# Optimization experiments

Measured on AMD Instinct MI355X. Metric: run time of the kernel, lower is better.

Reference implementation:

```python
import jax, jax.numpy as jnp
import numpy as np

J = 25
C_IN, HID, LAT = 3, 64, 32


def _graph_conv(x, A, W, b):
    # x: [N,T,J,Cin]; A: [J,J]; W: [Cin,Cout]; b: [Cout]
    A = jax.nn.softmax(A, axis=-1)
    # fused adjacency mix + projection: (A @ x) @ W + b
    x = jnp.einsum('ij,ntjc->ntic', A, x)
    return jnp.einsum('ntjc,cd->ntjd', x, W) + b


def setup_inputs() -> dict:
    key = jax.random.key(0)
    ks = jax.random.split(key, 13)
    x = jax.random.normal(ks[0], (32, 2048, J, C_IN), dtype=jnp.float32)
    eye = jnp.eye(J, dtype=jnp.float32)
    def lin(kw, kb, cin, cout):
        W = jax.random.normal(kw, (cin, cout), dtype=jnp.float32) / np.sqrt(cin)
        b = jax.random.normal(kb, (cout,), dtype=jnp.float32) * 0.01
        return W, b
    W1, b1 = lin(ks[1], ks[2], C_IN, HID)
    W2, b2 = lin(ks[3], ks[4], HID, LAT)
    W3, b3 = lin(ks[5], ks[6], LAT, HID)
    W4, b4 = lin(ks[7], ks[8], HID, C_IN)
    return {
        'x': x,
        'A1': eye, 'W1': W1, 'b1': b1,
        'A2': eye, 'W2': W2, 'b2': b2,
        'A3': eye, 'W3': W3, 'b3': b3,
        'A4': eye, 'W4': W4, 'b4': b4,
    }


def reference(x, A1, W1, b1, A2, W2, b2, A3, W3, b3, A4, W4, b4):
    h = jax.nn.relu(_graph_conv(x, A1, W1, b1))     # encoder_g1 + relu
    z = _graph_conv(h, A2, W2, b2)                  # encoder_g2 (no relu)
    h_dec = jax.nn.relu(_graph_conv(z, A3, W3, b3)) # decoder_g1 + relu
    out = _graph_conv(h_dec, A4, W4, b4)            # decoder_g2
    return out
```

## Files before the change

### kernel.cpp

```cpp
#include <hip/hip_runtime.h>
#include <math.h>

#define J 25
#define NJC 75
#define NWAVE 4
#define NTHREADS 256
#define NFPW 4
#define SCRW 2112

#define O_A1T  0
#define O_APP  1024
#define O_A4B  2048
#define O_W2T  3072
#define O_W3T  5120
#define O_W1T  7168
#define O_W4C  8192
#define O_B4   8512
#define O_BPPF 8576

using bf16x2 = __attribute__((ext_vector_type(2))) __bf16;
using bf16x8 = __attribute__((ext_vector_type(8))) __bf16;
using f32x4  = __attribute__((ext_vector_type(4))) float;
using f32x16 = __attribute__((ext_vector_type(16))) float;

__device__ inline bf16x8 zero8() {
    bf16x8 z;
    #pragma unroll
    for (int j = 0; j < 8; j++) z[j] = (__bf16)0.f;
    return z;
}

#if defined(__has_builtin)
#if __has_builtin(__builtin_amdgcn_cvt_pk_bf16_f32)
#define HAVE_PK_BF16 1
#endif
#endif

__device__ inline bf16x2 cvt2(float a, float b) {
#ifdef HAVE_PK_BF16
    return __builtin_amdgcn_cvt_pk_bf16_f32(a, b);
#else
    bf16x2 r; r[0] = (__bf16)a; r[1] = (__bf16)b; return r;
#endif
}
__device__ inline bf16x8 pk8(const f32x16& acc, int st) {
    const int b = 8 * st;
    bf16x8 r;
    #pragma unroll
    for (int p = 0; p < 4; p++) {
        bf16x2 v = cvt2(acc[b + 2 * p], acc[b + 2 * p + 1]);
        r[2 * p] = v[0]; r[2 * p + 1] = v[1];
    }
    return r;
}


__global__ void gcn_precompute(
    const float* __restrict__ A1, const float* __restrict__ W1, const float* __restrict__ b1,
    const float* __restrict__ A2, const float* __restrict__ W2, const float* __restrict__ b2,
    const float* __restrict__ A3, const float* __restrict__ W3, const float* __restrict__ b3,
    const float* __restrict__ A4, const float* __restrict__ W4, const float* __restrict__ b4,
    __bf16* __restrict__ cw)
{
    __shared__ float T[3125];
    __shared__ float bpp[64];
    float* T0 = T;        float* T1 = T + 625;  float* T2 = T + 1250;
    float* T3 = T + 1875; float* T4 = T + 2500;
    const int t = threadIdx.x;

    if (t < 100) {
        const int m = t / J, i = t % J;
        const float* Asrc = (m == 0) ? A1 : (m == 1) ? A2 : (m == 2) ? A3 : A4;
        float row[J];
        float mx = -1e30f;
        #pragma unroll
        for (int j = 0; j < J; j++) { row[j] = Asrc[i * J + j]; mx = fmaxf(mx, row[j]); }
        float s = 0.f;
        #pragma unroll
        for (int j = 0; j < J; j++) { row[j] = __expf(row[j] - mx); s += row[j]; }
        const float inv = 1.f / s;
        float* dst = T + m * 625 + i * J;
        #pragma unroll
        for (int j = 0; j < J; j++) dst[j] = row[j] * inv;
    }
    if (t < 64) {
        float s = b3[t];
        #pragma unroll
        for (int l = 0; l < 32; l++) s += W3[l * 64 + t] * b2[l];
        bpp[t] = s;
    }
    __syncthreads();

    for (int idx = t; idx < 625; idx += 256) {
        const int i = idx / J, jj = idx % J;
        float s = 0.f;
        #pragma unroll
        for (int k = 0; k < J; k++) s += T2[i * J + k] * T1[k * J + jj];
        T4[idx] = s;
    }
    __syncthreads();

    for (int i = t; i < 1024; i += 256) {
        const int b = i >> 8, n = (i >> 3) & 31, jj = i & 7;
        const int kn = 8 * b + jj;
        cw[O_A1T + i] = (__bf16)((kn < J && n < J) ? T0[n * J + kn] : 0.f);
        const int s = b >> 1, h = b & 1, r = 8 * s + jj;
        const int k32 = (r & 3) + 8 * (r >> 2) + 4 * h;
        cw[O_APP + i] = (__bf16)((k32 < J && n < J) ? T4[n * J + k32] : 0.f);
        cw[O_A4B + i] = (__bf16)((k32 < J && n < J) ? T3[n * J + k32] : 0.f);
    }
    for (int i = t; i < 2048; i += 256) {
        {
            const int b = i >> 8, n = (i >> 3) & 31, jj = i & 7;
            const int s = b >> 1, h = b & 1, r = 8 * (s & 1) + jj;
            const int d = 32 * (s >> 1) + (r & 3) + 8 * (r >> 2) + 4 * h;
            cw[O_W2T + i] = (__bf16)W2[d * 32 + n];
        }
        {
            const int tt = i >> 10, rr = i & 1023;
            const int b = rr >> 8, m = (rr >> 3) & 31, jj = rr & 7;
            const int s = b >> 1, h = b & 1, r = 8 * s + jj;
            const int l = (r & 3) + 8 * (r >> 2) + 4 * h;
            cw[O_W3T + i] = (__bf16)W3[l * 64 + tt * 32 + m];
        }
    }
    for (int i = t; i < 1024; i += 256) {
        const int tt = i >> 9, r = i & 511, hf = r >> 8, q = r & 255;
        const int m = q >> 3, c = q & 7, d = tt * 32 + m;
        float v = 0.f;
        if (hf == 0) {
            if (c < 3) v = W1[c * 64 + d];
            else if (c == 3) v = b1[d];
        }
        cw[O_W1T + i] = (__bf16)v;
    }
    if (t < 256) {
        const int c = t >> 6, b = (t >> 3) & 7, jj = t & 7;
        const int s = b >> 1, h = b & 1, r = 8 * (s & 1) + jj;
        const int d = 32 * (s >> 1) + (r & 3) + 8 * (r >> 2) + 4 * h;
        cw[O_W4C + t] = (c < 3) ? (__bf16)W4[d * 3 + c] : (__bf16)0.f;
    }
    {
        float* fwB = (float*)(cw + O_BPPF);
        if (t < 64) {
            const int g = t >> 4, h = (t >> 3) & 1, jj = t & 7;
            const int tt = g >> 1, st = g & 1;
            const int row32 = (jj & 3) + 16 * st + 8 * (jj >> 2) + 4 * h;
            fwB[t] = bpp[tt * 32 + row32];
        }
    }
    float* fb4 = (float*)(cw + O_B4);
    if (t >= 64 && t < 68) fb4[t - 64] = (t < 67) ? b4[t - 64] : 0.f;
}

__global__ __launch_bounds__(NTHREADS, 2) void gcn_fused(
    const float* __restrict__ x,
    const __bf16* __restrict__ cw,
    float* __restrict__ out)
{
    __shared__ __align__(16) __bf16 SCR[NWAVE * SCRW];

    const int t = threadIdx.x;
    const int w = t >> 6, lane = t & 63, ln = lane & 31, half = lane >> 5;
    const int fo = ln * 8;
    __bf16* scr = &SCR[w * SCRW];

    const long fbase = ((long)blockIdx.x * NWAVE + w) * NFPW;

    #pragma unroll
    for (int r = 0; r < 2; r++) {
        __bf16* s = scr + r * 1056;
        if (half == 0) s[(ln >> 3) * 264 + 24 + (ln & 7)] = (ln < J) ? (__bf16)1.f : (__bf16)0.f;
        if (lane < 21) s[3 * 264 + (lane / 7) * 8 + 1 + (lane % 7)] = (__bf16)0.f;
    }

    const int c0 = lane % 3, j0 = lane / 3;
    const int sx0 = (j0 >> 3) * 264 + c0 * 8 + (j0 & 7);
    const int i1 = 64 + lane, c1 = i1 % 3, j1 = i1 / 3;
    const int sx1 = (j1 >> 3) * 264 + c1 * 8 + (j1 & 7);

    {
        const long xb = fbase * NJC;
        float v0 = x[xb + lane];
        float v1 = (lane < NJC - 64) ? x[xb + 64 + lane] : 0.f;
        scr[sx0] = (__bf16)v0;
        if (lane < NJC - 64) scr[sx1] = (__bf16)v1;
    }
    float xv0 = 0.f, xv1 = 0.f;
    if (NFPW > 1) {
        const long xb = (fbase + 1) * NJC;
        xv0 = x[xb + lane];
        if (lane < NJC - 64) xv1 = x[xb + 64 + lane];
    }

    bf16x8 rA1T[2], rApp[2], rA4b[2], rW1[2], rW2[4], rW3[4], rW4[4];
    #pragma unroll
    for (int ks = 0; ks < 2; ks++) {
        rA1T[ks] = *(const bf16x8*)&cw[O_A1T + (2 * ks + half) * 256 + fo];
        rApp[ks] = *(const bf16x8*)&cw[O_APP + (2 * ks + half) * 256 + fo];
        rA4b[ks] = *(const bf16x8*)&cw[O_A4B + (2 * ks + half) * 256 + fo];
        rW1[ks]  = *(const bf16x8*)&cw[O_W1T + ks * 512 + half * 256 + fo];
    }
    #pragma unroll
    for (int ks = 0; ks < 4; ks++)
        rW2[ks] = *(const bf16x8*)&cw[O_W2T + (half + 2 * ks) * 256 + fo];
    #pragma unroll
    for (int tt = 0; tt < 2; tt++)
        #pragma unroll
        for (int ks = 0; ks < 2; ks++)
            rW3[tt * 2 + ks] = *(const bf16x8*)&cw[O_W3T + tt * 1024 + (half + 2 * ks) * 256 + fo];
    #pragma unroll
    for (int ks = 0; ks < 4; ks++) {
        rW4[ks] = zero8();
        if (ln < 3) rW4[ks] = *(const bf16x8*)&cw[O_W4C + ln * 64 + (half + 2 * ks) * 8];
    }
    f32x4 rBq[8];
    {
        const float* fwB = (const float*)(cw + O_BPPF);
        #pragma unroll
        for (int g = 0; g < 4; g++)
            #pragma unroll
            for (int p = 0; p < 2; p++)
                rBq[g * 2 + p] = *(const f32x4*)&fwB[(g * 2 + half) * 8 + 4 * p];
    }
    float b4v = 0.f;
    if (ln < 3) b4v = ((const float*)(cw + O_B4))[ln];

    f32x16 Z;
    #pragma unroll
    for (int z = 0; z < 16; z++) Z[z] = 0.f;

    for (int fi = 0; fi < NFPW; fi++) {
        const long f = fbase + fi;
        __bf16* sc = scr + (fi & 1) * 1056;

        if (fi + 1 < NFPW) {
            __bf16* sn = scr + ((fi + 1) & 1) * 1056;
            sn[sx0] = (__bf16)xv0;
            if (lane < NJC - 64) sn[sx1] = (__bf16)xv1;
        }
        if (fi + 2 < NFPW) {
            const long nxb = (f + 2) * NJC;
            xv0 = x[nxb + lane];
            if (lane < NJC - 64) xv1 = x[nxb + 64 + lane];
        }

        bf16x8 a0 = *(const bf16x8*)&sc[half * 264 + fo];
        bf16x8 a1 = *(const bf16x8*)&sc[(2 + half) * 264 + fo];
        f32x16 accY = __builtin_amdgcn_mfma_f32_32x32x16_bf16(a0, rA1T[0], Z, 0, 0, 0);
        accY = __builtin_amdgcn_mfma_f32_32x32x16_bf16(a1, rA1T[1], accY, 0, 0, 0);

        bf16x8 yb = zero8();
        if (half == 0) {
            bf16x2 q0 = cvt2(accY[0], accY[1]);
            bf16x2 q1 = cvt2(accY[2], accY[3]);
            yb[0] = q0[0]; yb[1] = q0[1]; yb[2] = q1[0]; yb[3] = q1[1];
        }
        bf16x8 hf[4];
        #pragma unroll
        for (int tt = 0; tt < 2; tt++) {
            f32x16 acc = __builtin_amdgcn_mfma_f32_32x32x16_bf16(rW1[tt], yb, Z, 0, 0, 0);
            #pragma unroll
            for (int z = 0; z < 16; z++) acc[z] = fmaxf(acc[z], 0.f);
            hf[2 * tt]     = pk8(acc, 0);
            hf[2 * tt + 1] = pk8(acc, 1);
        }

        f32x16 accU = __builtin_amdgcn_mfma_f32_32x32x16_bf16(hf[0], rW2[0], Z, 0, 0, 0);
        #pragma unroll
        for (int s = 1; s < 4; s++)
            accU = __builtin_amdgcn_mfma_f32_32x32x16_bf16(hf[s], rW2[s], accU, 0, 0, 0);
        bf16x8 uf[2] = { pk8(accU, 0), pk8(accU, 1) };

        f32x16 accV = __builtin_amdgcn_mfma_f32_32x32x16_bf16(uf[0], rApp[0], Z, 0, 0, 0);
        accV = __builtin_amdgcn_mfma_f32_32x32x16_bf16(uf[1], rApp[1], accV, 0, 0, 0);
        bf16x8 vf[2] = { pk8(accV, 0), pk8(accV, 1) };

        bf16x8 hd[4];
        #pragma unroll
        for (int tt = 0; tt < 2; tt++) {
            f32x16 acc = __builtin_amdgcn_mfma_f32_32x32x16_bf16(rW3[tt * 2 + 0], vf[0], Z, 0, 0, 0);
            acc = __builtin_amdgcn_mfma_f32_32x32x16_bf16(rW3[tt * 2 + 1], vf[1], acc, 0, 0, 0);
            #pragma unroll
            for (int st = 0; st < 2; st++) {
                const int g = 2 * tt + st;
                #pragma unroll
                for (int jj = 0; jj < 8; jj++)
                    acc[8 * st + jj] = fmaxf(acc[8 * st + jj] + rBq[g * 2 + (jj >> 2)][jj & 3], 0.f);
                hd[g] = pk8(acc, st);
            }
        }

        f32x16 accP = __builtin_amdgcn_mfma_f32_32x32x16_bf16(hd[0], rW4[0], Z, 0, 0, 0);
        #pragma unroll
        for (int s = 1; s < 4; s++)
            accP = __builtin_amdgcn_mfma_f32_32x32x16_bf16(hd[s], rW4[s], accP, 0, 0, 0);
        bf16x8 pf[2] = { pk8(accP, 0), pk8(accP, 1) };

        f32x16 accO = __builtin_amdgcn_mfma_f32_32x32x16_bf16(rA4b[0], pf[0], Z, 0, 0, 0);
        accO = __builtin_amdgcn_mfma_f32_32x32x16_bf16(rA4b[1], pf[1], accO, 0, 0, 0);
        if (ln < 3) {
            const long ob = f * NJC;
            #pragma unroll
            for (int r = 0; r < 16; r++) {
                const int row = (r & 3) + 8 * (r >> 2) + 4 * half;
                if (row < J) out[ob + row * 3 + ln] = accO[r] + b4v;
            }
        }
    }
}

extern "C" void kernel_launch(void* const* d_in, const int* in_sizes, int n_in,
                              void* d_out, int out_size, void* d_ws, size_t ws_size,
                              hipStream_t stream)
{
    const float* x  = (const float*)d_in[0];
    const float* A1 = (const float*)d_in[1];
    const float* W1 = (const float*)d_in[2];
    const float* b1 = (const float*)d_in[3];
    const float* A2 = (const float*)d_in[4];
    const float* W2 = (const float*)d_in[5];
    const float* b2 = (const float*)d_in[6];
    const float* A3 = (const float*)d_in[7];
    const float* W3 = (const float*)d_in[8];
    const float* b3 = (const float*)d_in[9];
    const float* A4 = (const float*)d_in[10];
    const float* W4 = (const float*)d_in[11];
    const float* b4 = (const float*)d_in[12];
    float* out = (float*)d_out;
    __bf16* cw = (__bf16*)d_ws;

    const int NT = in_sizes[0] / NJC;
    const int nblocks = NT / (NWAVE * NFPW);

    gcn_precompute<<<1, 256, 0, stream>>>(
        A1, W1, b1, A2, W2, b2, A3, W3, b3, A4, W4, b4, cw);
    gcn_fused<<<nblocks, NTHREADS, 0, stream>>>(x, cw, out);
}
```

Before: 149.0 us.

## Fuse weight precompute into main kernel and interleave two frames per iteration

Removes the separate single-block precompute kernel: every block now computes the softmaxed adjacencies and the repacked bf16 weights into shared memory itself, which saves a launch and its serialization. The main loop handles two frames per iteration with interleaved independent MFMA chains to hide MFMA latency, and frames per wave rise from 4 to 16 with a 4-frame double-buffered scratch, cutting the block count. In exchange each block redoes the small precompute, and register and LDS pressure grow, which can lower occupancy.

Result: faster. 143.8 us (-3.5%).

```diff
diff --git a/kernel.cpp b/kernel.cpp
--- a/kernel.cpp
+++ b/kernel.cpp
@@ -5,8 +5,9 @@
 #define NJC 75
 #define NWAVE 4
 #define NTHREADS 256
-#define NFPW 4
-#define SCRW 2112
+#define NFPW 16
+#define FRSZ 1056
+#define SCRW (4 * FRSZ)
 
 #define O_A1T  0
 #define O_APP  1024
@@ -17,6 +18,7 @@
 #define O_W4C  8192
 #define O_B4   8512
 #define O_BPPF 8576
+#define CWS_SZ 8704
 
 using bf16x2 = __attribute__((ext_vector_type(2))) __bf16;
 using bf16x8 = __attribute__((ext_vector_type(8))) __bf16;
@@ -54,113 +56,111 @@
     return r;
 }
 
-
-__global__ void gcn_precompute(
+__global__ __launch_bounds__(NTHREADS, 2) void gcn_fused(
+    const float* __restrict__ x,
     const float* __restrict__ A1, const float* __restrict__ W1, const float* __restrict__ b1,
     const float* __restrict__ A2, const float* __restrict__ W2, const float* __restrict__ b2,
     const float* __restrict__ A3, const float* __restrict__ W3, const float* __restrict__ b3,
     const float* __restrict__ A4, const float* __restrict__ W4, const float* __restrict__ b4,
-    __bf16* __restrict__ cw)
-{
-    __shared__ float T[3125];
-    __shared__ float bpp[64];
-    float* T0 = T;        float* T1 = T + 625;  float* T2 = T + 1250;
-    float* T3 = T + 1875; float* T4 = T + 2500;
-    const int t = threadIdx.x;
-
-    if (t < 100) {
-        const int m = t / J, i = t % J;
-        const float* Asrc = (m == 0) ? A1 : (m == 1) ? A2 : (m == 2) ? A3 : A4;
-        float row[J];
-        float mx = -1e30f;
-        #pragma unroll
-        for (int j = 0; j < J; j++) { row[j] = Asrc[i * J + j]; mx = fmaxf(mx, row[j]); }
-        float s = 0.f;
-        #pragma unroll
-        for (int j = 0; j < J; j++) { row[j] = __expf(row[j] - mx); s += row[j]; }
-        const float inv = 1.f / s;
-        float* dst = T + m * 625 + i * J;
-        #pragma unroll
-        for (int j = 0; j < J; j++) dst[j] = row[j] * inv;
-    }
-    if (t < 64) {
-        float s = b3[t];
-        #pragma unroll
-        for (int l = 0; l < 32; l++) s += W3[l * 64 + t] * b2[l];
-        bpp[t] = s;
-    }
-    __syncthreads();
-
-    for (int idx = t; idx < 625; idx += 256) {
-        const int i = idx / J, jj = idx % J;
-        float s = 0.f;
-        #pragma unroll
-        for (int k = 0; k < J; k++) s += T2[i * J + k] * T1[k * J + jj];
-        T4[idx] = s;
-    }
-    __syncthreads();
-
-    for (int i = t; i < 1024; i += 256) {
-        const int b = i >> 8, n = (i >> 3) & 31, jj = i & 7;
-        const int kn = 8 * b + jj;
-        cw[O_A1T + i] = (__bf16)((kn < J && n < J) ? T0[n * J + kn] : 0.f);
-        const int s = b >> 1, h = b & 1, r = 8 * s + jj;
-        const int k32 = (r & 3) + 8 * (r >> 2) + 4 * h;
-        cw[O_APP + i] = (__bf16)((k32 < J && n < J) ? T4[n * J + k32] : 0.f);
-        cw[O_A4B + i] = (__bf16)((k32 < J && n < J) ? T3[n * J + k32] : 0.f);
-    }
-    for (int i = t; i < 2048; i += 256) {
-        {
-            const int b = i >> 8, n = (i >> 3) & 31, jj = i & 7;
-            const int s = b >> 1, h = b & 1, r = 8 * (s & 1) + jj;
-            const int d = 32 * (s >> 1) + (r & 3) + 8 * (r >> 2) + 4 * h;
-            cw[O_W2T + i] = (__bf16)W2[d * 32 + n];
-        }
-        {
-            const int tt = i >> 10, rr = i & 1023;
-            const int b = rr >> 8, m = (rr >> 3) & 31, jj = rr & 7;
-            const int s = b >> 1, h = b & 1, r = 8 * s + jj;
-            const int l = (r & 3) + 8 * (r >> 2) + 4 * h;
-            cw[O_W3T + i] = (__bf16)W3[l * 64 + tt * 32 + m];
-        }
-    }
-    for (int i = t; i < 1024; i += 256) {
-        const int tt = i >> 9, r = i & 511, hf = r >> 8, q = r & 255;
-        const int m = q >> 3, c = q & 7, d = tt * 32 + m;
-        float v = 0.f;
-        if (hf == 0) {
-            if (c < 3) v = W1[c * 64 + d];
-            else if (c == 3) v = b1[d];
-        }
-        cw[O_W1T + i] = (__bf16)v;
-    }
-    if (t < 256) {
-        const int c = t >> 6, b = (t >> 3) & 7, jj = t & 7;
-        const int s = b >> 1, h = b & 1, r = 8 * (s & 1) + jj;
-        const int d = 32 * (s >> 1) + (r & 3) + 8 * (r >> 2) + 4 * h;
-        cw[O_W4C + t] = (c < 3) ? (__bf16)W4[d * 3 + c] : (__bf16)0.f;
-    }
-    {
-        float* fwB = (float*)(cw + O_BPPF);
-        if (t < 64) {
-            const int g = t >> 4, h = (t >> 3) & 1, jj = t & 7;
-            const int tt = g >> 1, st = g & 1;
-            const int row32 = (jj & 3) + 16 * st + 8 * (jj >> 2) + 4 * h;
-            fwB[t] = bpp[tt * 32 + row32];
-        }
-    }
-    float* fb4 = (float*)(cw + O_B4);
-    if (t >= 64 && t < 68) fb4[t - 64] = (t < 67) ? b4[t - 64] : 0.f;
-}
-
-__global__ __launch_bounds__(NTHREADS, 2) void gcn_fused(
-    const float* __restrict__ x,
-    const __bf16* __restrict__ cw,
     float* __restrict__ out)
 {
     __shared__ __align__(16) __bf16 SCR[NWAVE * SCRW];
+    __shared__ __align__(16) __bf16 CWS[CWS_SZ];
 
     const int t = threadIdx.x;
+
+    {
+        float* T   = (float*)SCR;
+        float* bpp = T + 3125;
+        float* T0 = T;        float* T1 = T + 625;  float* T2 = T + 1250;
+        float* T3 = T + 1875; float* T4 = T + 2500;
+
+        if (t < 100) {
+            const int m = t / J, i = t % J;
+            const float* Asrc = (m == 0) ? A1 : (m == 1) ? A2 : (m == 2) ? A3 : A4;
+            float row[J];
+            float mx = -1e30f;
+            #pragma unroll
+            for (int j = 0; j < J; j++) { row[j] = Asrc[i * J + j]; mx = fmaxf(mx, row[j]); }
+            float s = 0.f;
+            #pragma unroll
+            for (int j = 0; j < J; j++) { row[j] = __expf(row[j] - mx); s += row[j]; }
+            const float inv = 1.f / s;
+            float* dst = T + m * 625 + i * J;
+            #pragma unroll
+            for (int j = 0; j < J; j++) dst[j] = row[j] * inv;
+        }
+        if (t < 64) {
+            float s = b3[t];
+            #pragma unroll
+            for (int l = 0; l < 32; l++) s += W3[l * 64 + t] * b2[l];
+            bpp[t] = s;
+        }
+        __syncthreads();
+
+        for (int idx = t; idx < 625; idx += 256) {
+            const int i = idx / J, jj = idx % J;
+            float s = 0.f;
+            #pragma unroll
+            for (int k = 0; k < J; k++) s += T2[i * J + k] * T1[k * J + jj];
+            T4[idx] = s;
+        }
+        __syncthreads();
+
+        for (int i = t; i < 1024; i += 256) {
+            const int b = i >> 8, n = (i >> 3) & 31, jj = i & 7;
+            const int kn = 8 * b + jj;
+            CWS[O_A1T + i] = (__bf16)((kn < J && n < J) ? T0[n * J + kn] : 0.f);
+            const int s = b >> 1, h = b & 1, r = 8 * s + jj;
+            const int k32 = (r & 3) + 8 * (r >> 2) + 4 * h;
+            CWS[O_APP + i] = (__bf16)((k32 < J && n < J) ? T4[n * J + k32] : 0.f);
+            CWS[O_A4B + i] = (__bf16)((k32 < J && n < J) ? T3[n * J + k32] : 0.f);
+        }
+        for (int i = t; i < 2048; i += 256) {
+            {
+                const int b = i >> 8, n = (i >> 3) & 31, jj = i & 7;
+                const int s = b >> 1, h = b & 1, r = 8 * (s & 1) + jj;
+                const int d = 32 * (s >> 1) + (r & 3) + 8 * (r >> 2) + 4 * h;
+                CWS[O_W2T + i] = (__bf16)W2[d * 32 + n];
+            }
+            {
+                const int tt = i >> 10, rr = i & 1023;
+                const int b = rr >> 8, m = (rr >> 3) & 31, jj = rr & 7;
+                const int s = b >> 1, h = b & 1, r = 8 * s + jj;
+                const int l = (r & 3) + 8 * (r >> 2) + 4 * h;
+                CWS[O_W3T + i] = (__bf16)W3[l * 64 + tt * 32 + m];
+            }
+        }
+        for (int i = t; i < 1024; i += 256) {
+            const int tt = i >> 9, rq = i & 511, hf = rq >> 8, q = rq & 255;
+            const int m = q >> 3, c = q & 7, d = tt * 32 + m;
+            float v = 0.f;
+            if (hf == 0) {
+                if (c < 3) v = W1[c * 64 + d];
+                else if (c == 3) v = b1[d];
+            }
+            CWS[O_W1T + i] = (__bf16)v;
+        }
+        {
+            const int c = t >> 6, b = (t >> 3) & 7, jj = t & 7;
+            const int s = b >> 1, h = b & 1, r = 8 * (s & 1) + jj;
+            const int d = 32 * (s >> 1) + (r & 3) + 8 * (r >> 2) + 4 * h;
+            CWS[O_W4C + t] = (c < 3) ? (__bf16)W4[d * 3 + c] : (__bf16)0.f;
+        }
+        {
+            float* fwB = (float*)(CWS + O_BPPF);
+            if (t < 64) {
+                const int g = t >> 4, h = (t >> 3) & 1, jj = t & 7;
+                const int tt = g >> 1, st = g & 1;
+                const int row32 = (jj & 3) + 16 * st + 8 * (jj >> 2) + 4 * h;
+                fwB[t] = bpp[tt * 32 + row32];
+            }
+            float* fb4 = (float*)(CWS + O_B4);
+            if (t >= 64 && t < 68) fb4[t - 64] = (t < 67) ? b4[t - 64] : 0.f;
+        }
+        __syncthreads();
+    }
+
     const int w = t >> 6, lane = t & 63, ln = lane & 31, half = lane >> 5;
     const int fo = ln * 8;
     __bf16* scr = &SCR[w * SCRW];
@@ -168,8 +168,8 @@
     const long fbase = ((long)blockIdx.x * NWAVE + w) * NFPW;
 
     #pragma unroll
-    for (int r = 0; r < 2; r++) {
-        __bf16* s = scr + r * 1056;
+    for (int r = 0; r < 4; r++) {
+        __bf16* s = scr + r * FRSZ;
         if (half == 0) s[(ln >> 3) * 264 + 24 + (ln & 7)] = (ln < J) ? (__bf16)1.f : (__bf16)0.f;
         if (lane < 21) s[3 * 264 + (lane / 7) * 8 + 1 + (lane % 7)] = (__bf16)0.f;
     }
@@ -179,44 +179,47 @@
     const int i1 = 64 + lane, c1 = i1 % 3, j1 = i1 / 3;
     const int sx1 = (j1 >> 3) * 264 + c1 * 8 + (j1 & 7);
 
-    {
-        const long xb = fbase * NJC;
-        float v0 = x[xb + lane];
-        float v1 = (lane < NJC - 64) ? x[xb + 64 + lane] : 0.f;
-        scr[sx0] = (__bf16)v0;
-        if (lane < NJC - 64) scr[sx1] = (__bf16)v1;
-    }
-    float xv0 = 0.f, xv1 = 0.f;
-    if (NFPW > 1) {
-        const long xb = (fbase + 1) * NJC;
-        xv0 = x[xb + lane];
-        if (lane < NJC - 64) xv1 = x[xb + 64 + lane];
+    #pragma unroll
+    for (int u = 0; u < 2; u++) {
+        const long xb = (fbase + u) * NJC;
+        __bf16* s = scr + u * FRSZ;
+        s[sx0] = (__bf16)x[xb + lane];
+        if (lane < NJC - 64) s[sx1] = (__bf16)x[xb + 64 + lane];
+    }
+    float nx0a = 0.f, nx1a = 0.f, nx0b = 0.f, nx1b = 0.f;
+    if (NFPW > 2) {
+        const long xb2 = (fbase + 2) * NJC;
+        nx0a = x[xb2 + lane];
+        if (lane < NJC - 64) nx1a = x[xb2 + 64 + lane];
+        const long xb3 = (fbase + 3) * NJC;
+        nx0b = x[xb3 + lane];
+        if (lane < NJC - 64) nx1b = x[xb3 + 64 + lane];
     }
 
     bf16x8 rA1T[2], rApp[2], rA4b[2], rW1[2], rW2[4], rW3[4], rW4[4];
     #pragma unroll
     for (int ks = 0; ks < 2; ks++) {
-        rA1T[ks] = *(const bf16x8*)&cw[O_A1T + (2 * ks + half) * 256 + fo];
-        rApp[ks] = *(const bf16x8*)&cw[O_APP + (2 * ks + half) * 256 + fo];
-        rA4b[ks] = *(const bf16x8*)&cw[O_A4B + (2 * ks + half) * 256 + fo];
-        rW1[ks]  = *(const bf16x8*)&cw[O_W1T + ks * 512 + half * 256 + fo];
+        rA1T[ks] = *(const bf16x8*)&CWS[O_A1T + (2 * ks + half) * 256 + fo];
+        rApp[ks] = *(const bf16x8*)&CWS[O_APP + (2 * ks + half) * 256 + fo];
+        rA4b[ks] = *(const bf16x8*)&CWS[O_A4B + (2 * ks + half) * 256 + fo];
+        rW1[ks]  = *(const bf16x8*)&CWS[O_W1T + ks * 512 + half * 256 + fo];
     }
     #pragma unroll
     for (int ks = 0; ks < 4; ks++)
-        rW2[ks] = *(const bf16x8*)&cw[O_W2T + (half + 2 * ks) * 256 + fo];
+        rW2[ks] = *(const bf16x8*)&CWS[O_W2T + (half + 2 * ks) * 256 + fo];
     #pragma unroll
     for (int tt = 0; tt < 2; tt++)
         #pragma unroll
         for (int ks = 0; ks < 2; ks++)
-            rW3[tt * 2 + ks] = *(const bf16x8*)&cw[O_W3T + tt * 1024 + (half + 2 * ks) * 256 + fo];
+            rW3[tt * 2 + ks] = *(const bf16x8*)&CWS[O_W3T + tt * 1024 + (half + 2 * ks) * 256 + fo];
     #pragma unroll
     for (int ks = 0; ks < 4; ks++) {
         rW4[ks] = zero8();
-        if (ln < 3) rW4[ks] = *(const bf16x8*)&cw[O_W4C + ln * 64 + (half + 2 * ks) * 8];
+        if (ln < 3) rW4[ks] = *(const bf16x8*)&CWS[O_W4C + ln * 64 + (half + 2 * ks) * 8];
     }
     f32x4 rBq[8];
     {
-        const float* fwB = (const float*)(cw + O_BPPF);
+        const float* fwB = (const float*)(CWS + O_BPPF);
         #pragma unroll
         for (int g = 0; g < 4; g++)
             #pragma unroll
@@ -224,87 +227,126 @@
                 rBq[g * 2 + p] = *(const f32x4*)&fwB[(g * 2 + half) * 8 + 4 * p];
     }
     float b4v = 0.f;
-    if (ln < 3) b4v = ((const float*)(cw + O_B4))[ln];
+    if (ln < 3) b4v = ((const float*)(CWS + O_B4))[ln];
 
     f32x16 Z;
     #pragma unroll
     for (int z = 0; z < 16; z++) Z[z] = 0.f;
 
-    for (int fi = 0; fi < NFPW; fi++) {
-        const long f = fbase + fi;
-        __bf16* sc = scr + (fi & 1) * 1056;
-
-        if (fi + 1 < NFPW) {
-            __bf16* sn = scr + ((fi + 1) & 1) * 1056;
-            sn[sx0] = (__bf16)xv0;
-            if (lane < NJC - 64) sn[sx1] = (__bf16)xv1;
-        }
+    for (int fi = 0; fi < NFPW; fi += 2) {
+        const long fA = fbase + fi;
+        const int pcur = (fi >> 1) & 1;
+        __bf16* scA = scr + pcur * (2 * FRSZ);
+        __bf16* scB = scA + FRSZ;
+
         if (fi + 2 < NFPW) {
-            const long nxb = (f + 2) * NJC;
-            xv0 = x[nxb + lane];
-            if (lane < NJC - 64) xv1 = x[nxb + 64 + lane];
-        }
-
-        bf16x8 a0 = *(const bf16x8*)&sc[half * 264 + fo];
-        bf16x8 a1 = *(const bf16x8*)&sc[(2 + half) * 264 + fo];
-        f32x16 accY = __builtin_amdgcn_mfma_f32_32x32x16_bf16(a0, rA1T[0], Z, 0, 0, 0);
-        accY = __builtin_amdgcn_mfma_f32_32x32x16_bf16(a1, rA1T[1], accY, 0, 0, 0);
-
-        bf16x8 yb = zero8();
+            __bf16* snA = scr + (pcur ^ 1) * (2 * FRSZ);
+            __bf16* snB = snA + FRSZ;
+            snA[sx0] = (__bf16)nx0a;
+            if (lane < NJC - 64) snA[sx1] = (__bf16)nx1a;
+            snB[sx0] = (__bf16)nx0b;
+            if (lane < NJC - 64) snB[sx1] = (__bf16)nx1b;
+        }
+        if (fi + 4 < NFPW) {
+            const long xbA = (fA + 4) * NJC;
+            nx0a = x[xbA + lane];
+            if (lane < NJC - 64) nx1a = x[xbA + 64 + lane];
+            const long xbB = (fA + 5) * NJC;
+            nx0b = x[xbB + lane];
+            if (lane < NJC - 64) nx1b = x[xbB + 64 + lane];
+        }
+
+        bf16x8 a0A = *(const bf16x8*)&scA[half * 264 + fo];
+        bf16x8 a1A = *(const bf16x8*)&scA[(2 + half) * 264 + fo];
+        bf16x8 a0B = *(const bf16x8*)&scB[half * 264 + fo];
+        bf16x8 a1B = *(const bf16x8*)&scB[(2 + half) * 264 + fo];
+        f32x16 accYA = __builtin_amdgcn_mfma_f32_32x32x16_bf16(a0A, rA1T[0], Z, 0, 0, 0);
+        f32x16 accYB = __builtin_amdgcn_mfma_f32_32x32x16_bf16(a0B, rA1T[0], Z, 0, 0, 0);
+        accYA = __builtin_amdgcn_mfma_f32_32x32x16_bf16(a1A, rA1T[1], accYA, 0, 0, 0);
+        accYB = __builtin_amdgcn_mfma_f32_32x32x16_bf16(a1B, rA1T[1], accYB, 0, 0, 0);
+
+        bf16x8 ybA = zero8(), ybB = zero8();
         if (half == 0) {
-            bf16x2 q0 = cvt2(accY[0], accY[1]);
-            bf16x2 q1 = cvt2(accY[2], accY[3]);
-            yb[0] = q0[0]; yb[1] = q0[1]; yb[2] = q1[0]; yb[3] = q1[1];
-        }
-        bf16x8 hf[4];
+            bf16x2 q0 = cvt2(accYA[0], accYA[1]);
+            bf16x2 q1 = cvt2(accYA[2], accYA[3]);
+            ybA[0] = q0[0]; ybA[1] = q0[1]; ybA[2] = q1[0]; ybA[3] = q1[1];
+            q0 = cvt2(accYB[0], accYB[1]);
+            q1 = cvt2(accYB[2], accYB[3]);
+            ybB[0] = q0[0]; ybB[1] = q0[1]; ybB[2] = q1[0]; ybB[3] = q1[1];
+        }
+        bf16x8 hfA[4], hfB[4];
         #pragma unroll
         for (int tt = 0; tt < 2; tt++) {
-            f32x16 acc = __builtin_amdgcn_mfma_f32_32x32x16_bf16(rW1[tt], yb, Z, 0, 0, 0);
-            #pragma unroll
-            for (int z = 0; z < 16; z++) acc[z] = fmaxf(acc[z], 0.f);
-            hf[2 * tt]     = pk8(acc, 0);
-            hf[2 * tt + 1] = pk8(acc, 1);
-        }
-
-        f32x16 accU = __builtin_amdgcn_mfma_f32_32x32x16_bf16(hf[0], rW2[0], Z, 0, 0, 0);
-        #pragma unroll
-        for (int s = 1; s < 4; s++)
-            accU = __builtin_amdgcn_mfma_f32_32x32x16_bf16(hf[s], rW2[s], accU, 0, 0, 0);
-        bf16x8 uf[2] = { pk8(accU, 0), pk8(accU, 1) };
-
-        f32x16 accV = __builtin_amdgcn_mfma_f32_32x32x16_bf16(uf[0], rApp[0], Z, 0, 0, 0);
-        accV = __builtin_amdgcn_mfma_f32_32x32x16_bf16(uf[1], rApp[1], accV, 0, 0, 0);
-        bf16x8 vf[2] = { pk8(accV, 0), pk8(accV, 1) };
-
-        bf16x8 hd[4];
+            f32x16 aA = __builtin_amdgcn_mfma_f32_32x32x16_bf16(rW1[tt], ybA, Z, 0, 0, 0);
+            f32x16 aB = __builtin_amdgcn_mfma_f32_32x32x16_bf16(rW1[tt], ybB, Z, 0, 0, 0);
+            #pragma unroll
+            for (int z = 0; z < 16; z++) { aA[z] = fmaxf(aA[z], 0.f); aB[z] = fmaxf(aB[z], 0.f); }
+            hfA[2 * tt]     = pk8(aA, 0);
+            hfA[2 * tt + 1] = pk8(aA, 1);
+            hfB[2 * tt]     = pk8(aB, 0);
+            hfB[2 * tt + 1] = pk8(aB, 1);
+        }
+
+        f32x16 accUA = __builtin_amdgcn_mfma_f32_32x32x16_bf16(hfA[0], rW2[0], Z, 0, 0, 0);
+        f32x16 accUB = __builtin_amdgcn_mfma_f32_32x32x16_bf16(hfB[0], rW2[0], Z, 0, 0, 0);
+        #pragma unroll
+        for (int s = 1; s < 4; s++) {
+            accUA = __builtin_amdgcn_mfma_f32_32x32x16_bf16(hfA[s], rW2[s], accUA, 0, 0, 0);
+            accUB = __builtin_amdgcn_mfma_f32_32x32x16_bf16(hfB[s], rW2[s], accUB, 0, 0, 0);
+        }
+        bf16x8 ufA[2] = { pk8(accUA, 0), pk8(accUA, 1) };
+        bf16x8 ufB[2] = { pk8(accUB, 0), pk8(accUB, 1) };
+
+        f32x16 accVA = __builtin_amdgcn_mfma_f32_32x32x16_bf16(ufA[0], rApp[0], Z, 0, 0, 0);
+        f32x16 accVB = __builtin_amdgcn_mfma_f32_32x32x16_bf16(ufB[0], rApp[0], Z, 0, 0, 0);
+        accVA = __builtin_amdgcn_mfma_f32_32x32x16_bf16(ufA[1], rApp[1], accVA, 0, 0, 0);
+        accVB = __builtin_amdgcn_mfma_f32_32x32x16_bf16(ufB[1], rApp[1], accVB, 0, 0, 0);
+        bf16x8 vfA[2] = { pk8(accVA, 0), pk8(accVA, 1) };
+        bf16x8 vfB[2] = { pk8(accVB, 0), pk8(accVB, 1) };
+
+        bf16x8 hdA[4], hdB[4];
         #pragma unroll
         for (int tt = 0; tt < 2; tt++) {
-            f32x16 acc = __builtin_amdgcn_mfma_f32_32x32x16_bf16(rW3[tt * 2 + 0], vf[0], Z, 0, 0, 0);
-            acc = __builtin_amdgcn_mfma_f32_32x32x16_bf16(rW3[tt * 2 + 1], vf[1], acc, 0, 0, 0);
+            f32x16 aA = __builtin_amdgcn_mfma_f32_32x32x16_bf16(rW3[tt * 2 + 0], vfA[0], Z, 0, 0, 0);
+            f32x16 aB = __builtin_amdgcn_mfma_f32_32x32x16_bf16(rW3[tt * 2 + 0], vfB[0], Z, 0, 0, 0);
+            aA = __builtin_amdgcn_mfma_f32_32x32x16_bf16(rW3[tt * 2 + 1], vfA[1], aA, 0, 0, 0);
+            aB = __builtin_amdgcn_mfma_f32_32x32x16_bf16(rW3[tt * 2 + 1], vfB[1], aB, 0, 0, 0);
             #pragma unroll
             for (int st = 0; st < 2; st++) {
                 const int g = 2 * tt + st;
                 #pragma unroll
-                for (int jj = 0; jj < 8; jj++)
-                    acc[8 * st + jj] = fmaxf(acc[8 * st + jj] + rBq[g * 2 + (jj >> 2)][jj & 3], 0.f);
-                hd[g] = pk8(acc, st);
-            }
-        }
-
-        f32x16 accP = __builtin_amdgcn_mfma_f32_32x32x16_bf16(hd[0], rW4[0], Z, 0, 0, 0);
-        #pragma unroll
-        for (int s = 1; s < 4; s++)
-            accP = __builtin_amdgcn_mfma_f32_32x32x16_bf16(hd[s], rW4[s], accP, 0, 0, 0);
-        bf16x8 pf[2] = { pk8(accP, 0), pk8(accP, 1) };
-
-        f32x16 accO = __builtin_amdgcn_mfma_f32_32x32x16_bf16(rA4b[0], pf[0], Z, 0, 0, 0);
-        accO = __builtin_amdgcn_mfma_f32_32x32x16_bf16(rA4b[1], pf[1], accO, 0, 0, 0);
+                for (int jj = 0; jj < 8; jj++) {
+                    aA[8 * st + jj] = fmaxf(aA[8 * st + jj] + rBq[g * 2 + (jj >> 2)][jj & 3], 0.f);
+                    aB[8 * st + jj] = fmaxf(aB[8 * st + jj] + rBq[g * 2 + (jj >> 2)][jj & 3], 0.f);
+                }
+                hdA[g] = pk8(aA, st);
+                hdB[g] = pk8(aB, st);
+            }
+        }
+
+        f32x16 accPA = __builtin_amdgcn_mfma_f32_32x32x16_bf16(hdA[0], rW4[0], Z, 0, 0, 0);
+        f32x16 accPB = __builtin_amdgcn_mfma_f32_32x32x16_bf16(hdB[0], rW4[0], Z, 0, 0, 0);
+        #pragma unroll
+        for (int s = 1; s < 4; s++) {
+            accPA = __builtin_amdgcn_mfma_f32_32x32x16_bf16(hdA[s], rW4[s], accPA, 0, 0, 0);
+            accPB = __builtin_amdgcn_mfma_f32_32x32x16_bf16(hdB[s], rW4[s], accPB, 0, 0, 0);
+        }
+        bf16x8 pfA[2] = { pk8(accPA, 0), pk8(accPA, 1) };
+        bf16x8 pfB[2] = { pk8(accPB, 0), pk8(accPB, 1) };
+
+        f32x16 accOA = __builtin_amdgcn_mfma_f32_32x32x16_bf16(rA4b[0], pfA[0], Z, 0, 0, 0);
+        f32x16 accOB = __builtin_amdgcn_mfma_f32_32x32x16_bf16(rA4b[0], pfB[0], Z, 0, 0, 0);
+        accOA = __builtin_amdgcn_mfma_f32_32x32x16_bf16(rA4b[1], pfA[1], accOA, 0, 0, 0);
+        accOB = __builtin_amdgcn_mfma_f32_32x32x16_bf16(rA4b[1], pfB[1], accOB, 0, 0, 0);
         if (ln < 3) {
-            const long ob = f * NJC;
+            const long obA = fA * NJC, obB = obA + NJC;
             #pragma unroll
             for (int r = 0; r < 16; r++) {
                 const int row = (r & 3) + 8 * (r >> 2) + 4 * half;
-                if (row < J) out[ob + row * 3 + ln] = accO[r] + b4v;
+                if (row < J) {
+                    out[obA + row * 3 + ln] = accOA[r] + b4v;
+                    out[obB + row * 3 + ln] = accOB[r] + b4v;
+                }
             }
         }
     }
@@ -328,12 +370,11 @@
     const float* W4 = (const float*)d_in[11];
     const float* b4 = (const float*)d_in[12];
     float* out = (float*)d_out;
-    __bf16* cw = (__bf16*)d_ws;
+    (void)d_ws; (void)ws_size;
 
     const int NT = in_sizes[0] / NJC;
     const int nblocks = NT / (NWAVE * NFPW);
 
-    gcn_precompute<<<1, 256, 0, stream>>>(
-        A1, W1, b1, A2, W2, b2, A3, W3, b3, A4, W4, b4, cw);
-    gcn_fused<<<nblocks, NTHREADS, 0, stream>>>(x, cw, out);
-}
+    gcn_fused<<<nblocks, NTHREADS, 0, stream>>>(
+        x, A1, W1, b1, A2, W2, b2, A3, W3, b3, A4, W4, b4, out);
+}
```

## Fold weight precompute into fused kernel, stage weights in LDS, fold bias into MFMA

Applied to the files above, without the earlier changes.

Removes the separate single-block precompute launch. Every block of the main kernel now recomputes the softmaxed adjacencies and the packed bf16 weights into shared memory. W2/W3 fragments are reloaded from LDS per frame instead of being held in registers, which frees registers so occupancy can rise (launch bounds 2 -> 3 blocks/CU). Frames per wave double from 4 to 8, and the decoder bias is preloaded as the MFMA accumulator initial value. The trade-off is redundant per-block setup work (global reads plus a 25x25 matmul per block), added LDS traffic per frame, and fewer blocks.

Result: no change. 147.5 us (-1.0%).

```diff
diff --git a/kernel.cpp b/kernel.cpp
--- a/kernel.cpp
+++ b/kernel.cpp
@@ -5,8 +5,9 @@
 #define NJC 75
 #define NWAVE 4
 #define NTHREADS 256
-#define NFPW 4
-#define SCRW 2112
+#define NFPW 8
+#define FRSZ 1056
+#define SCRW (2 * FRSZ)
 
 #define O_A1T  0
 #define O_APP  1024
@@ -17,6 +18,7 @@
 #define O_W4C  8192
 #define O_B4   8512
 #define O_BPPF 8576
+#define CWS_SZ 8704
 
 using bf16x2 = __attribute__((ext_vector_type(2))) __bf16;
 using bf16x8 = __attribute__((ext_vector_type(8))) __bf16;
@@ -54,113 +56,111 @@
     return r;
 }
 
-
-__global__ void gcn_precompute(
+__global__ __launch_bounds__(NTHREADS, 3) void gcn_fused(
+    const float* __restrict__ x,
     const float* __restrict__ A1, const float* __restrict__ W1, const float* __restrict__ b1,
     const float* __restrict__ A2, const float* __restrict__ W2, const float* __restrict__ b2,
     const float* __restrict__ A3, const float* __restrict__ W3, const float* __restrict__ b3,
     const float* __restrict__ A4, const float* __restrict__ W4, const float* __restrict__ b4,
-    __bf16* __restrict__ cw)
-{
-    __shared__ float T[3125];
-    __shared__ float bpp[64];
-    float* T0 = T;        float* T1 = T + 625;  float* T2 = T + 1250;
-    float* T3 = T + 1875; float* T4 = T + 2500;
-    const int t = threadIdx.x;
-
-    if (t < 100) {
-        const int m = t / J, i = t % J;
-        const float* Asrc = (m == 0) ? A1 : (m == 1) ? A2 : (m == 2) ? A3 : A4;
-        float row[J];
-        float mx = -1e30f;
-        #pragma unroll
-        for (int j = 0; j < J; j++) { row[j] = Asrc[i * J + j]; mx = fmaxf(mx, row[j]); }
-        float s = 0.f;
-        #pragma unroll
-        for (int j = 0; j < J; j++) { row[j] = __expf(row[j] - mx); s += row[j]; }
-        const float inv = 1.f / s;
-        float* dst = T + m * 625 + i * J;
-        #pragma unroll
-        for (int j = 0; j < J; j++) dst[j] = row[j] * inv;
-    }
-    if (t < 64) {
-        float s = b3[t];
-        #pragma unroll
-        for (int l = 0; l < 32; l++) s += W3[l * 64 + t] * b2[l];
-        bpp[t] = s;
-    }
-    __syncthreads();
-
-    for (int idx = t; idx < 625; idx += 256) {
-        const int i = idx / J, jj = idx % J;
-        float s = 0.f;
-        #pragma unroll
-        for (int k = 0; k < J; k++) s += T2[i * J + k] * T1[k * J + jj];
-        T4[idx] = s;
-    }
-    __syncthreads();
-
-    for (int i = t; i < 1024; i += 256) {
-        const int b = i >> 8, n = (i >> 3) & 31, jj = i & 7;
-        const int kn = 8 * b + jj;
-        cw[O_A1T + i] = (__bf16)((kn < J && n < J) ? T0[n * J + kn] : 0.f);
-        const int s = b >> 1, h = b & 1, r = 8 * s + jj;
-        const int k32 = (r & 3) + 8 * (r >> 2) + 4 * h;
-        cw[O_APP + i] = (__bf16)((k32 < J && n < J) ? T4[n * J + k32] : 0.f);
-        cw[O_A4B + i] = (__bf16)((k32 < J && n < J) ? T3[n * J + k32] : 0.f);
-    }
-    for (int i = t; i < 2048; i += 256) {
-        {
-            const int b = i >> 8, n = (i >> 3) & 31, jj = i & 7;
-            const int s = b >> 1, h = b & 1, r = 8 * (s & 1) + jj;
-            const int d = 32 * (s >> 1) + (r & 3) + 8 * (r >> 2) + 4 * h;
-            cw[O_W2T + i] = (__bf16)W2[d * 32 + n];
-        }
-        {
-            const int tt = i >> 10, rr = i & 1023;
-            const int b = rr >> 8, m = (rr >> 3) & 31, jj = rr & 7;
-            const int s = b >> 1, h = b & 1, r = 8 * s + jj;
-            const int l = (r & 3) + 8 * (r >> 2) + 4 * h;
-            cw[O_W3T + i] = (__bf16)W3[l * 64 + tt * 32 + m];
-        }
-    }
-    for (int i = t; i < 1024; i += 256) {
-        const int tt = i >> 9, r = i & 511, hf = r >> 8, q = r & 255;
-        const int m = q >> 3, c = q & 7, d = tt * 32 + m;
-        float v = 0.f;
-        if (hf == 0) {
-            if (c < 3) v = W1[c * 64 + d];
-            else if (c == 3) v = b1[d];
-        }
-        cw[O_W1T + i] = (__bf16)v;
-    }
-    if (t < 256) {
-        const int c = t >> 6, b = (t >> 3) & 7, jj = t & 7;
-        const int s = b >> 1, h = b & 1, r = 8 * (s & 1) + jj;
-        const int d = 32 * (s >> 1) + (r & 3) + 8 * (r >> 2) + 4 * h;
-        cw[O_W4C + t] = (c < 3) ? (__bf16)W4[d * 3 + c] : (__bf16)0.f;
-    }
-    {
-        float* fwB = (float*)(cw + O_BPPF);
-        if (t < 64) {
-            const int g = t >> 4, h = (t >> 3) & 1, jj = t & 7;
-            const int tt = g >> 1, st = g & 1;
-            const int row32 = (jj & 3) + 16 * st + 8 * (jj >> 2) + 4 * h;
-            fwB[t] = bpp[tt * 32 + row32];
-        }
-    }
-    float* fb4 = (float*)(cw + O_B4);
-    if (t >= 64 && t < 68) fb4[t - 64] = (t < 67) ? b4[t - 64] : 0.f;
-}
-
-__global__ __launch_bounds__(NTHREADS, 2) void gcn_fused(
-    const float* __restrict__ x,
-    const __bf16* __restrict__ cw,
     float* __restrict__ out)
 {
     __shared__ __align__(16) __bf16 SCR[NWAVE * SCRW];
+    __shared__ __align__(16) __bf16 CWS[CWS_SZ];
 
     const int t = threadIdx.x;
+
+    {
+        float* T   = (float*)SCR;
+        float* bpp = T + 3125;
+        float* T0 = T;        float* T1 = T + 625;  float* T2 = T + 1250;
+        float* T3 = T + 1875; float* T4 = T + 2500;
+
+        if (t < 100) {
+            const int m = t / J, i = t % J;
+            const float* Asrc = (m == 0) ? A1 : (m == 1) ? A2 : (m == 2) ? A3 : A4;
+            float row[J];
+            float mx = -1e30f;
+            #pragma unroll
+            for (int j = 0; j < J; j++) { row[j] = Asrc[i * J + j]; mx = fmaxf(mx, row[j]); }
+            float s = 0.f;
+            #pragma unroll
+            for (int j = 0; j < J; j++) { row[j] = __expf(row[j] - mx); s += row[j]; }
+            const float inv = 1.f / s;
+            float* dst = T + m * 625 + i * J;
+            #pragma unroll
+            for (int j = 0; j < J; j++) dst[j] = row[j] * inv;
+        }
+        if (t < 64) {
+            float s = b3[t];
+            #pragma unroll
+            for (int l = 0; l < 32; l++) s += W3[l * 64 + t] * b2[l];
+            bpp[t] = s;
+        }
+        __syncthreads();
+
+        for (int idx = t; idx < 625; idx += 256) {
+            const int i = idx / J, jj = idx % J;
+            float s = 0.f;
+            #pragma unroll
+            for (int k = 0; k < J; k++) s += T2[i * J + k] * T1[k * J + jj];
+            T4[idx] = s;
+        }
+        __syncthreads();
+
+        for (int i = t; i < 1024; i += 256) {
+            const int b = i >> 8, n = (i >> 3) & 31, jj = i & 7;
+            const int kn = 8 * b + jj;
+            CWS[O_A1T + i] = (__bf16)((kn < J && n < J) ? T0[n * J + kn] : 0.f);
+            const int s = b >> 1, h = b & 1, r = 8 * s + jj;
+            const int k32 = (r & 3) + 8 * (r >> 2) + 4 * h;
+            CWS[O_APP + i] = (__bf16)((k32 < J && n < J) ? T4[n * J + k32] : 0.f);
+            CWS[O_A4B + i] = (__bf16)((k32 < J && n < J) ? T3[n * J + k32] : 0.f);
+        }
+        for (int i = t; i < 2048; i += 256) {
+            {
+                const int b = i >> 8, n = (i >> 3) & 31, jj = i & 7;
+                const int s = b >> 1, h = b & 1, r = 8 * (s & 1) + jj;
+                const int d = 32 * (s >> 1) + (r & 3) + 8 * (r >> 2) + 4 * h;
+                CWS[O_W2T + i] = (__bf16)W2[d * 32 + n];
+            }
+            {
+                const int tt = i >> 10, rr = i & 1023;
+                const int b = rr >> 8, m = (rr >> 3) & 31, jj = rr & 7;
+                const int s = b >> 1, h = b & 1, r = 8 * s + jj;
+                const int l = (r & 3) + 8 * (r >> 2) + 4 * h;
+                CWS[O_W3T + i] = (__bf16)W3[l * 64 + tt * 32 + m];
+            }
+        }
+        for (int i = t; i < 1024; i += 256) {
+            const int tt = i >> 9, rq = i & 511, hf = rq >> 8, q = rq & 255;
+            const int m = q >> 3, c = q & 7, d = tt * 32 + m;
+            float v = 0.f;
+            if (hf == 0) {
+                if (c < 3) v = W1[c * 64 + d];
+                else if (c == 3) v = b1[d];
+            }
+            CWS[O_W1T + i] = (__bf16)v;
+        }
+        {
+            const int c = t >> 6, b = (t >> 3) & 7, jj = t & 7;
+            const int s = b >> 1, h = b & 1, r = 8 * (s & 1) + jj;
+            const int d = 32 * (s >> 1) + (r & 3) + 8 * (r >> 2) + 4 * h;
+            CWS[O_W4C + t] = (c < 3) ? (__bf16)W4[d * 3 + c] : (__bf16)0.f;
+        }
+        {
+            float* fwB = (float*)(CWS + O_BPPF);
+            if (t < 64) {
+                const int g = t >> 4, h = (t >> 3) & 1, jj = t & 7;
+                const int tt = g >> 1, st = g & 1;
+                const int row32 = (jj & 3) + 16 * st + 8 * (jj >> 2) + 4 * h;
+                fwB[t] = bpp[tt * 32 + row32];
+            }
+            float* fb4 = (float*)(CWS + O_B4);
+            if (t >= 64 && t < 68) fb4[t - 64] = (t < 67) ? b4[t - 64] : 0.f;
+        }
+        __syncthreads();
+    }
+
     const int w = t >> 6, lane = t & 63, ln = lane & 31, half = lane >> 5;
     const int fo = ln * 8;
     __bf16* scr = &SCR[w * SCRW];
@@ -169,7 +169,7 @@
 
     #pragma unroll
     for (int r = 0; r < 2; r++) {
-        __bf16* s = scr + r * 1056;
+        __bf16* s = scr + r * FRSZ;
         if (half == 0) s[(ln >> 3) * 264 + 24 + (ln & 7)] = (ln < J) ? (__bf16)1.f : (__bf16)0.f;
         if (lane < 21) s[3 * 264 + (lane / 7) * 8 + 1 + (lane % 7)] = (__bf16)0.f;
     }
@@ -193,38 +193,37 @@
         if (lane < NJC - 64) xv1 = x[xb + 64 + lane];
     }
 
-    bf16x8 rA1T[2], rApp[2], rA4b[2], rW1[2], rW2[4], rW3[4], rW4[4];
+    bf16x8 rA1T[2], rApp[2], rA4b[2], rW1[2], rW4[4];
     #pragma unroll
     for (int ks = 0; ks < 2; ks++) {
-        rA1T[ks] = *(const bf16x8*)&cw[O_A1T + (2 * ks + half) * 256 + fo];
-        rApp[ks] = *(const bf16x8*)&cw[O_APP + (2 * ks + half) * 256 + fo];
-        rA4b[ks] = *(const bf16x8*)&cw[O_A4B + (2 * ks + half) * 256 + fo];
-        rW1[ks]  = *(const bf16x8*)&cw[O_W1T + ks * 512 + half * 256 + fo];
-    }
-    #pragma unroll
-    for (int ks = 0; ks < 4; ks++)
-        rW2[ks] = *(const bf16x8*)&cw[O_W2T + (half + 2 * ks) * 256 + fo];
-    #pragma unroll
-    for (int tt = 0; tt < 2; tt++)
-        #pragma unroll
-        for (int ks = 0; ks < 2; ks++)
-            rW3[tt * 2 + ks] = *(const bf16x8*)&cw[O_W3T + tt * 1024 + (half + 2 * ks) * 256 + fo];
+        rA1T[ks] = *(const bf16x8*)&CWS[O_A1T + (2 * ks + half) * 256 + fo];
+        rApp[ks] = *(const bf16x8*)&CWS[O_APP + (2 * ks + half) * 256 + fo];
+        rA4b[ks] = *(const bf16x8*)&CWS[O_A4B + (2 * ks + half) * 256 + fo];
+        rW1[ks]  = *(const bf16x8*)&CWS[O_W1T + ks * 512 + half * 256 + fo];
+    }
     #pragma unroll
     for (int ks = 0; ks < 4; ks++) {
         rW4[ks] = zero8();
-        if (ln < 3) rW4[ks] = *(const bf16x8*)&cw[O_W4C + ln * 64 + (half + 2 * ks) * 8];
-    }
-    f32x4 rBq[8];
+        if (ln < 3) rW4[ks] = *(const bf16x8*)&CWS[O_W4C + ln * 64 + (half + 2 * ks) * 8];
+    }
+    f32x16 rB16[2];
     {
-        const float* fwB = (const float*)(cw + O_BPPF);
-        #pragma unroll
-        for (int g = 0; g < 4; g++)
-            #pragma unroll
-            for (int p = 0; p < 2; p++)
-                rBq[g * 2 + p] = *(const f32x4*)&fwB[(g * 2 + half) * 8 + 4 * p];
+        const float* fwB = (const float*)(CWS + O_BPPF);
+        #pragma unroll
+        for (int tt = 0; tt < 2; tt++)
+            #pragma unroll
+            for (int st = 0; st < 2; st++) {
+                f32x4 qa = *(const f32x4*)&fwB[32 * tt + 16 * st + 8 * half + 0];
+                f32x4 qb = *(const f32x4*)&fwB[32 * tt + 16 * st + 8 * half + 4];
+                #pragma unroll
+                for (int j = 0; j < 4; j++) {
+                    rB16[tt][8 * st + j]     = qa[j];
+                    rB16[tt][8 * st + 4 + j] = qb[j];
+                }
+            }
     }
     float b4v = 0.f;
-    if (ln < 3) b4v = ((const float*)(cw + O_B4))[ln];
+    if (ln < 3) b4v = ((const float*)(CWS + O_B4))[ln];
 
     f32x16 Z;
     #pragma unroll
@@ -232,10 +231,10 @@
 
     for (int fi = 0; fi < NFPW; fi++) {
         const long f = fbase + fi;
-        __bf16* sc = scr + (fi & 1) * 1056;
+        __bf16* sc = scr + (fi & 1) * FRSZ;
 
         if (fi + 1 < NFPW) {
-            __bf16* sn = scr + ((fi + 1) & 1) * 1056;
+            __bf16* sn = scr + ((fi + 1) & 1) * FRSZ;
             sn[sx0] = (__bf16)xv0;
             if (lane < NJC - 64) sn[sx1] = (__bf16)xv1;
         }
@@ -249,6 +248,11 @@
         bf16x8 a1 = *(const bf16x8*)&sc[(2 + half) * 264 + fo];
         f32x16 accY = __builtin_amdgcn_mfma_f32_32x32x16_bf16(a0, rA1T[0], Z, 0, 0, 0);
         accY = __builtin_amdgcn_mfma_f32_32x32x16_bf16(a1, rA1T[1], accY, 0, 0, 0);
+
+        bf16x8 w2f[4];
+        #pragma unroll
+        for (int s = 0; s < 4; s++)
+            w2f[s] = *(const bf16x8*)&CWS[O_W2T + (half + 2 * s) * 256 + fo];
 
         bf16x8 yb = zero8();
         if (half == 0) {
@@ -266,11 +270,18 @@
             hf[2 * tt + 1] = pk8(acc, 1);
         }
 
-        f32x16 accU = __builtin_amdgcn_mfma_f32_32x32x16_bf16(hf[0], rW2[0], Z, 0, 0, 0);
+        f32x16 accU = __builtin_amdgcn_mfma_f32_32x32x16_bf16(hf[0], w2f[0], Z, 0, 0, 0);
         #pragma unroll
         for (int s = 1; s < 4; s++)
-            accU = __builtin_amdgcn_mfma_f32_32x32x16_bf16(hf[s], rW2[s], accU, 0, 0, 0);
+            accU = __builtin_amdgcn_mfma_f32_32x32x16_bf16(hf[s], w2f[s], accU, 0, 0, 0);
         bf16x8 uf[2] = { pk8(accU, 0), pk8(accU, 1) };
+
+        bf16x8 w3f[4];
+        #pragma unroll
+        for (int tt = 0; tt < 2; tt++)
+            #pragma unroll
+            for (int ks = 0; ks < 2; ks++)
+                w3f[tt * 2 + ks] = *(const bf16x8*)&CWS[O_W3T + tt * 1024 + (half + 2 * ks) * 256 + fo];
 
         f32x16 accV = __builtin_amdgcn_mfma_f32_32x32x16_bf16(uf[0], rApp[0], Z, 0, 0, 0);
         accV = __builtin_amdgcn_mfma_f32_32x32x16_bf16(uf[1], rApp[1], accV, 0, 0, 0);
@@ -279,16 +290,12 @@
         bf16x8 hd[4];
         #pragma unroll
         for (int tt = 0; tt < 2; tt++) {
-            f32x16 acc = __builtin_amdgcn_mfma_f32_32x32x16_bf16(rW3[tt * 2 + 0], vf[0], Z, 0, 0, 0);
-            acc = __builtin_amdgcn_mfma_f32_32x32x16_bf16(rW3[tt * 2 + 1], vf[1], acc, 0, 0, 0);
-            #pragma unroll
-            for (int st = 0; st < 2; st++) {
-                const int g = 2 * tt + st;
-                #pragma unroll
-                for (int jj = 0; jj < 8; jj++)
-                    acc[8 * st + jj] = fmaxf(acc[8 * st + jj] + rBq[g * 2 + (jj >> 2)][jj & 3], 0.f);
-                hd[g] = pk8(acc, st);
-            }
+            f32x16 acc = __builtin_amdgcn_mfma_f32_32x32x16_bf16(w3f[tt * 2 + 0], vf[0], rB16[tt], 0, 0, 0);
+            acc = __builtin_amdgcn_mfma_f32_32x32x16_bf16(w3f[tt * 2 + 1], vf[1], acc, 0, 0, 0);
+            #pragma unroll
+            for (int z = 0; z < 16; z++) acc[z] = fmaxf(acc[z], 0.f);
+            hd[2 * tt]     = pk8(acc, 0);
+            hd[2 * tt + 1] = pk8(acc, 1);
         }
 
         f32x16 accP = __builtin_amdgcn_mfma_f32_32x32x16_bf16(hd[0], rW4[0], Z, 0, 0, 0);
@@ -328,12 +335,11 @@
     const float* W4 = (const float*)d_in[11];
     const float* b4 = (const float*)d_in[12];
     float* out = (float*)d_out;
-    __bf16* cw = (__bf16*)d_ws;
+    (void)d_ws; (void)ws_size;
 
     const int NT = in_sizes[0] / NJC;
     const int nblocks = NT / (NWAVE * NFPW);
 
-    gcn_precompute<<<1, 256, 0, stream>>>(
-        A1, W1, b1, A2, W2, b2, A3, W3, b3, A4, W4, b4, cw);
-    gcn_fused<<<nblocks, NTHREADS, 0, stream>>>(x, cw, out);
-}
+    gcn_fused<<<nblocks, NTHREADS, 0, stream>>>(
+        x, A1, W1, b1, A2, W2, b2, A3, W3, b3, A4, W4, b4, out);
+}
```
